# Kernel tuning notes

Measured on AMD Instinct MI355X. Metric: run time of the kernel, lower is better.

The kernel has to match this reference:

```python
import jax, jax.numpy as jnp
import numpy as np

N = 524288          # total atoms (sorted by degree)
E = 1433600         # total directed bonds
B, L = 16384, 32    # molecules x atoms-per-molecule (B*L == N)
NODE, EDGE, H, OUT = 64, 16, 128, 128
N0 = 8192           # number of degree-0 atoms
DEG_COUNTS = {1: 65536, 2: 131072, 3: 196608, 4: 98304, 5: 24576}
BN_EPS = 1e-5


def setup_inputs() -> dict:
    key = jax.random.key(0)
    ks = jax.random.split(key, 24)
    inp = {}
    inp["node_feat"] = jax.random.normal(ks[0], (N, NODE), jnp.float32)
    inp["edge_feat"] = jax.random.normal(ks[1], (E, EDGE), jnp.float32)
    i = 2
    for d in (1, 2, 3, 4, 5):
        n_d = DEG_COUNTS[d]
        inp[f"nbr_node_d{d}"] = jax.random.randint(ks[i], (n_d, d), 0, N, jnp.int32); i += 1
        inp[f"nbr_edge_d{d}"] = jax.random.randint(ks[i], (n_d, d), 0, E, jnp.int32); i += 1
    inp["atom_index"] = jnp.arange(B * L, dtype=jnp.int32).reshape(B, L)

    def lin(k, o, fan_in):
        return jax.random.normal(k, (o, fan_in), jnp.float32) / np.sqrt(fan_in).astype(np.float32)

    inp["out_W0"] = lin(ks[12], OUT, NODE); inp["out_b0"] = jnp.zeros((OUT,), jnp.float32)
    inp["out_W1"] = lin(ks[13], OUT, H);    inp["out_b1"] = jnp.zeros((OUT,), jnp.float32)
    inp["out_W2"] = lin(ks[14], OUT, H);    inp["out_b2"] = jnp.zeros((OUT,), jnp.float32)
    inp["conv0_selfW"] = lin(ks[15], H, NODE)
    inp["conv0_degW"] = jax.random.normal(ks[16], (5, H, NODE + EDGE), jnp.float32) / np.sqrt(NODE + EDGE).astype(np.float32)
    inp["conv0_bias"] = jnp.zeros((1, H), jnp.float32)
    inp["conv1_selfW"] = lin(ks[17], H, H)
    inp["conv1_degW"] = jax.random.normal(ks[18], (5, H, H + EDGE), jnp.float32) / np.sqrt(H + EDGE).astype(np.float32)
    inp["conv1_bias"] = jnp.zeros((1, H), jnp.float32)
    return inp


def _graph_degree_conv(node_repr, edge_repr, selfW, degW, bias, nbr_nodes, nbr_edges):
    out_size = selfW.shape[0]
    # degree 0: zero neighbor contribution
    parts = [jnp.zeros((N0, out_size), node_repr.dtype)]
    for di, d in enumerate((1, 2, 3, 4, 5)):
        nn_rep = node_repr[nbr_nodes[di]]          # [n_d, d, node]
        ee_rep = edge_repr[nbr_edges[di]]          # [n_d, d, edge]
        summed = jnp.concatenate([nn_rep.sum(1), ee_rep.sum(1)], axis=-1)  # [n_d, node+edge]
        parts.append(summed @ degW[di].T)          # per-degree linear (no bias)
    neighbor_repr = jnp.concatenate(parts, axis=0)  # nodes sorted by degree -> aligned
    act = node_repr @ selfW.T + neighbor_repr + bias
    # BatchNorm1d(affine=False), training-mode batch stats (biased variance)
    mean = act.mean(0)
    var = act.var(0)
    act = (act - mean) / jnp.sqrt(var + BN_EPS)
    return jax.nn.relu(act)


def reference(node_feat, edge_feat,
              nbr_node_d1, nbr_edge_d1, nbr_node_d2, nbr_edge_d2,
              nbr_node_d3, nbr_edge_d3, nbr_node_d4, nbr_edge_d4,
              nbr_node_d5, nbr_edge_d5, atom_index,
              out_W0, out_b0, out_W1, out_b1, out_W2, out_b2,
              conv0_selfW, conv0_degW, conv0_bias,
              conv1_selfW, conv1_degW, conv1_bias):
    nbr_nodes = (nbr_node_d1, nbr_node_d2, nbr_node_d3, nbr_node_d4, nbr_node_d5)
    nbr_edges = (nbr_edge_d1, nbr_edge_d2, nbr_edge_d3, nbr_edge_d4, nbr_edge_d5)

    x = node_feat
    acc = jax.nn.softmax(x @ out_W0.T + out_b0, axis=1)
    x = _graph_degree_conv(x, edge_feat, conv0_selfW, conv0_degW, conv0_bias, nbr_nodes, nbr_edges)
    acc = acc + jax.nn.softmax(x @ out_W1.T + out_b1, axis=1)
    x = _graph_degree_conv(x, edge_feat, conv1_selfW, conv1_degW, conv1_bias, nbr_nodes, nbr_edges)
    acc = acc + jax.nn.softmax(x @ out_W2.T + out_b2, axis=1)
    # scatter per-atom activations into [batch, max_len, OUT]
    return acc[atom_index]
```

## Files before the change

### kernel.cpp

```cpp
#include <hip/hip_runtime.h>
#include <math.h>


typedef short  short8   __attribute__((ext_vector_type(8)));
typedef unsigned short ushort8v __attribute__((ext_vector_type(8)));
typedef float  f32x4    __attribute__((ext_vector_type(4)));
typedef unsigned int u32;

static constexpr int  N_ATOMS = 524288;
static constexpr long NROWCOL = (long)N_ATOMS * 128;
static constexpr int  NBLK    = N_ATOMS / 64;

__device__ __forceinline__ ushort f2bf(float x) {
    unsigned u = __float_as_uint(x);
    return (ushort)((u + 0x7fffu + ((u >> 16) & 1u)) >> 16);
}
__device__ __forceinline__ float bf2f(ushort h) {
    return __uint_as_float(((unsigned)h) << 16);
}

__device__ __forceinline__ void gload_lds16(const ushort* g, ushort* l) {
    __builtin_amdgcn_global_load_lds(
        (const __attribute__((address_space(1))) u32*)g,
        (__attribute__((address_space(3))) u32*)l, 16, 0, 0);
}

__device__ __forceinline__ void seg_of(long r, int& d, long& off) {
    if      (r < 73728)  { d = 1; off = 8192;  }
    else if (r < 204800) { d = 2; off = 73728; }
    else if (r < 401408) { d = 3; off = 204800;}
    else if (r < 499712) { d = 4; off = 401408;}
    else                 { d = 5; off = 499712;}
}

__device__ __forceinline__ uint4 pack8(const float v[8]) {
    uint4 w;
    w.x = f2bf(v[0]) | ((unsigned)f2bf(v[1]) << 16);
    w.y = f2bf(v[2]) | ((unsigned)f2bf(v[3]) << 16);
    w.z = f2bf(v[4]) | ((unsigned)f2bf(v[5]) << 16);
    w.w = f2bf(v[6]) | ((unsigned)f2bf(v[7]) << 16);
    return w;
}
__device__ __forceinline__ short8 pack8s(const float v[8]) {
    short8 o;
#pragma unroll
    for (int e = 0; e < 8; ++e) o[e] = (short)f2bf(v[e]);
    return o;
}

__global__ __launch_bounds__(256)
void esum_kernel(const float* __restrict__ edge_feat,
                 const int* __restrict__ ne1, const int* __restrict__ ne2,
                 const int* __restrict__ ne3, const int* __restrict__ ne4,
                 const int* __restrict__ ne5, ushort* __restrict__ esumb)
{
    const long t = (long)blockIdx.x * 256 + threadIdx.x;
    const long r = 8192 + (t >> 1);
    const int  h = (int)(t & 1);
    int d; long off; seg_of(r, d, off);
    const int* ne = (d==1)?ne1:(d==2)?ne2:(d==3)?ne3:(d==4)?ne4:ne5;
    const long i0 = (r - off) * d;
    float v[8] = {0,0,0,0,0,0,0,0};
    for (int j = 0; j < d; ++j) {
        const long e = ne[i0 + j];
        const float4* p = (const float4*)(edge_feat + e * 16 + h * 8);
        const float4 a = p[0], b = p[1];
        v[0]+=a.x; v[1]+=a.y; v[2]+=a.z; v[3]+=a.w;
        v[4]+=b.x; v[5]+=b.y; v[6]+=b.z; v[7]+=b.w;
    }
    *(uint4*)(esumb + (r - 8192) * 16 + h * 8) = pack8(v);
}

__global__ void wprep(const float* __restrict__ src, ushort* __restrict__ dst,
                      int rows, int Ks, int Kd)
{
    const int i = blockIdx.x * 256 + threadIdx.x;
    if (i >= rows * Kd) return;
    const int r = i / Kd, c = i % Kd;
    dst[i] = f2bf(c < Ks ? src[r * Ks + c] : 0.f);
}

__global__ void wprep_img(const float* __restrict__ src, ushort* __restrict__ dst, int K)
{
    const int i = blockIdx.x * 256 + threadIdx.x;
    if (i >= 128 * K) return;
    const int row = i / K, col = i % K;
    dst[(col >> 3) * 1024 + row * 8 + (col & 7)] = f2bf(src[i]);
}

template<int NG, bool F32, bool BN>
__device__ __forceinline__ void stage_rows(const void* Xv, long r0,
                                           ushort* __restrict__ Ab,
                                           const float* __restrict__ statsL)
{
    for (int t = threadIdx.x; t < 64 * NG; t += 256) {
        const int row = t / NG, g = t % NG;
        const long gr = r0 + row;
        float v[8];
        if (F32) {
            const float4* p = (const float4*)((const float*)Xv + gr * (long)(NG * 8) + g * 8);
            const float4 a = p[0], b = p[1];
            v[0]=a.x; v[1]=a.y; v[2]=a.z; v[3]=a.w;
            v[4]=b.x; v[5]=b.y; v[6]=b.z; v[7]=b.w;
        } else {
            const ushort8v u = *(const ushort8v*)((const ushort*)Xv + gr * (long)(NG * 8) + g * 8);
#pragma unroll
            for (int e = 0; e < 8; ++e) v[e] = bf2f(u[e]);
        }
        if (BN) {
            const int c0 = g * 8;
#pragma unroll
            for (int e = 0; e < 8; ++e)
                v[e] = fmaxf(0.f, (v[e] - statsL[c0 + e]) * statsL[128 + c0 + e]);
        }
        ((uint4*)Ab)[row * NG + (g ^ (row & 7))] = pack8(v);
    }
}

template<int NGL, int NST, int NGN, bool F32, bool BN>
__device__ __forceinline__ void stage_gather(const void* Xv,
                                             const ushort* __restrict__ esumb,
                                             const int* __restrict__ nnl, int d,
                                             long r0, ushort* __restrict__ Ab,
                                             const float* __restrict__ statsL)
{
    for (int t = threadIdx.x; t < 64 * NST; t += 256) {
        const int row = t / NST, g = t % NST;
        float v[8] = {0,0,0,0,0,0,0,0};
        if (g < NGN) {
            const int c0 = g * 8;
            for (int j = 0; j < d; ++j) {
                const long idx = nnl[row * d + j];
                if (F32) {
                    const float4* p = (const float4*)((const float*)Xv + idx * (long)(NGN * 8) + c0);
                    const float4 a = p[0], b = p[1];
                    v[0]+=a.x; v[1]+=a.y; v[2]+=a.z; v[3]+=a.w;
                    v[4]+=b.x; v[5]+=b.y; v[6]+=b.z; v[7]+=b.w;
                } else {
                    const ushort8v u = *(const ushort8v*)((const ushort*)Xv + idx * (long)(NGN * 8) + c0);
#pragma unroll
                    for (int e = 0; e < 8; ++e) {
                        float x = bf2f(u[e]);
                        if (BN) x = fmaxf(0.f, (x - statsL[c0 + e]) * statsL[128 + c0 + e]);
                        v[e] += x;
                    }
                }
            }
        } else if (g < NGN + 2) {
            const long er = r0 + row - 8192;
            const ushort8v u = *(const ushort8v*)(esumb + er * 16 + (g - NGN) * 8);
#pragma unroll
            for (int e = 0; e < 8; ++e) v[e] = bf2f(u[e]);
        }
        ((uint4*)Ab)[row * NGL + (g ^ (row & 7))] = pack8(v);
    }
}

template<int KS, int NG>
__device__ __forceinline__ void mfma_lds(const ushort* __restrict__ Ab,
                                         const ushort* __restrict__ Wb, int KP,
                                         int wc, f32x4 acc[4][2])
{
    const int lane = threadIdx.x & 63;
    const int lg = lane >> 4, lr = lane & 15;
#pragma unroll
    for (int ks = 0; ks < KS; ++ks) {
        short8 B0 = *(const short8*)(Wb + (long)(wc + lr) * KP + ks * 32 + 8 * lg);
        short8 B1 = *(const short8*)(Wb + (long)(wc + 16 + lr) * KP + ks * 32 + 8 * lg);
        const int gk = ks * 4 + lg;
#pragma unroll
        for (int m = 0; m < 4; ++m) {
            const int row = 16 * m + lr;
            const short8 a = *(const short8*)(Ab + (row * NG + (gk ^ (row & 7))) * 8);
            acc[m][0] = __builtin_amdgcn_mfma_f32_16x16x32_bf16(a, B0, acc[m][0], 0, 0, 0);
            acc[m][1] = __builtin_amdgcn_mfma_f32_16x16x32_bf16(a, B1, acc[m][1], 0, 0, 0);
        }
    }
}

template<int K1, bool A1F32, bool BNIN, int NGL2, int NST2, int NGN2, int KS2, int KP2>
__global__ __launch_bounds__(256, 2)
void conv_kernel(const void* __restrict__ X, const ushort* __restrict__ Wb1,
                 const ushort* __restrict__ Wb2base,
                 const int* __restrict__ nn1, const int* __restrict__ nn2,
                 const int* __restrict__ nn3, const int* __restrict__ nn4,
                 const int* __restrict__ nn5,
                 const ushort* __restrict__ esumb, const float* __restrict__ cbias,
                 const float* __restrict__ stats_in,
                 ushort* __restrict__ act_out, float* __restrict__ part)
{
    constexpr int NG1 = K1 / 8;
    constexpr int KS1 = K1 / 32;
    constexpr int NGMAX = (NGL2 > NG1) ? NGL2 : NG1;
    __shared__ uint4 AbV[64 * NGMAX];
    __shared__ int   nnl[320];
    __shared__ float statsL[256];
    ushort* Ab = (ushort*)AbV;

    const long r0 = (long)blockIdx.x * 64;
    const int wid = threadIdx.x >> 6, lane = threadIdx.x & 63;
    const int lg = lane >> 4, lr = lane & 15, wc = wid * 32;

    if (BNIN)
        for (int t = threadIdx.x; t < 256; t += 256) statsL[t] = stats_in[t];

    int d = 0;
    const bool has2 = (r0 >= 8192);
    if (has2) {
        long off; seg_of(r0, d, off);
        const int* nn = (d==1)?nn1:(d==2)?nn2:(d==3)?nn3:(d==4)?nn4:nn5;
        const long i0 = (r0 - off) * d;
        for (int t = threadIdx.x; t < 64 * d; t += 256) nnl[t] = nn[i0 + t];
    }
    __syncthreads();

    stage_rows<NG1, A1F32, BNIN>(X, r0, Ab, statsL);
    __syncthreads();
    f32x4 acc[4][2] = {};
    mfma_lds<KS1, NG1>(Ab, Wb1, K1, wc, acc);

    if (has2) {
        __syncthreads();
        stage_gather<NGL2, NST2, NGN2, A1F32, BNIN>(X, esumb, nnl, d, r0, Ab, statsL);
        __syncthreads();
        const ushort* Wb2 = Wb2base + (long)(d - 1) * 128 * KP2;
        mfma_lds<KS2, NGL2>(Ab, Wb2, KP2, wc, acc);
    }

#pragma unroll
    for (int n = 0; n < 2; ++n) {
        const float bv = cbias[wc + n * 16 + lr];
#pragma unroll
        for (int m = 0; m < 4; ++m)
#pragma unroll
            for (int j = 0; j < 4; ++j) acc[m][n][j] += bv;
    }
#pragma unroll
    for (int m = 0; m < 4; ++m)
#pragma unroll
        for (int j = 0; j < 4; ++j) {
            const long row = r0 + 16 * m + 4 * lg + j;
#pragma unroll
            for (int n = 0; n < 2; ++n)
                act_out[row * 128 + wc + n * 16 + lr] = f2bf(acc[m][n][j]);
        }
#pragma unroll
    for (int n = 0; n < 2; ++n) {
        float s = 0.f, q = 0.f;
#pragma unroll
        for (int m = 0; m < 4; ++m)
#pragma unroll
            for (int j = 0; j < 4; ++j) { const float v = acc[m][n][j]; s += v; q += v * v; }
        s += __shfl_xor(s, 16); s += __shfl_xor(s, 32);
        q += __shfl_xor(q, 16); q += __shfl_xor(q, 32);
        if (lane < 16) {
            part[(long)blockIdx.x * 256 + wc + n * 16 + lr]       = s;
            part[(long)blockIdx.x * 256 + 128 + wc + n * 16 + lr] = q;
        }
    }
}

__global__ __launch_bounds__(256)
void bn_finalize(const float* __restrict__ part, float* __restrict__ stats)
{
    const int c = blockIdx.x;
    float s = 0.f, q = 0.f;
    for (int b = threadIdx.x; b < NBLK; b += 256) {
        s += part[(long)b * 256 + c];
        q += part[(long)b * 256 + 128 + c];
    }
#pragma unroll
    for (int o = 1; o < 64; o <<= 1) { s += __shfl_xor(s, o); q += __shfl_xor(q, o); }
    __shared__ float rs[4], rq[4];
    const int wid = threadIdx.x >> 6;
    if ((threadIdx.x & 63) == 0) { rs[wid] = s; rq[wid] = q; }
    __syncthreads();
    if (threadIdx.x == 0) {
        s = rs[0] + rs[1] + rs[2] + rs[3];
        q = rq[0] + rq[1] + rq[2] + rq[3];
        const float mean = s * (1.0f / N_ATOMS);
        const float var  = q * (1.0f / N_ATOMS) - mean * mean;
        stats[c]       = mean;
        stats[128 + c] = 1.0f / sqrtf(var + 1e-5f);
    }
}

__device__ __forceinline__ void mfma8_img(const ushort* __restrict__ Wl, int base,
                                          int ks, int lg, int lr,
                                          short8 af, f32x4 (&acc)[8])
{
    const int a0 = base + (ks * 4 + lg) * 1024 + lr * 8;
#pragma unroll
    for (int n = 0; n < 8; ++n) {
        const short8 bf = *(const short8*)(Wl + a0 + n * 128);
        acc[n] = __builtin_amdgcn_mfma_f32_16x16x32_bf16(af, bf, acc[n], 0, 0, 0);
    }
}

__device__ __forceinline__ short8 cvt_bn(short8 u, int k0, const float* __restrict__ sl)
{
    float v[8];
#pragma unroll
    for (int e = 0; e < 8; ++e)
        v[e] = fmaxf(0.f, (bf2f((ushort)u[e]) - sl[k0 + e]) * sl[128 + k0 + e]);
    return pack8s(v);
}

__device__ __forceinline__ void softmax_accum(f32x4 (&acc)[8],
                                              const float* __restrict__ bias,
                                              int lr, f32x4 (&oacc)[8])
{
    float bb[8];
#pragma unroll
    for (int n = 0; n < 8; ++n) bb[n] = bias[n * 16 + lr];
#pragma unroll
    for (int j = 0; j < 4; ++j) {
        float mx = -1e30f;
#pragma unroll
        for (int n = 0; n < 8; ++n) { acc[n][j] += bb[n]; mx = fmaxf(mx, acc[n][j]); }
        mx = fmaxf(mx, __shfl_xor(mx, 1));
        mx = fmaxf(mx, __shfl_xor(mx, 2));
        mx = fmaxf(mx, __shfl_xor(mx, 4));
        mx = fmaxf(mx, __shfl_xor(mx, 8));
        float s = 0.f;
#pragma unroll
        for (int n = 0; n < 8; ++n) {
            const float e = __expf(acc[n][j] - mx);
            acc[n][j] = e; s += e;
        }
        s += __shfl_xor(s, 1); s += __shfl_xor(s, 2);
        s += __shfl_xor(s, 4); s += __shfl_xor(s, 8);
        const float inv = 1.0f / s;
#pragma unroll
        for (int n = 0; n < 8; ++n) oacc[n][j] += acc[n][j] * inv;
    }
}

__global__ __launch_bounds__(256, 2)
void out_kernel(const float* __restrict__ node, const ushort* __restrict__ act0b,
                const ushort* __restrict__ act1b, const ushort* __restrict__ wimg,
                const float* __restrict__ b0, const float* __restrict__ b1,
                const float* __restrict__ b2,
                const float* __restrict__ stats0, const float* __restrict__ stats1,
                float* __restrict__ out)
{
    __shared__ ushort Wlds[24576];
    __shared__ float sl[512];

    const int wid = threadIdx.x >> 6, lane = threadIdx.x & 63;
    const int lg = lane >> 4, lr = lane & 15;
    const long rA = (long)blockIdx.x * 64 + wid * 16 + lr;

#pragma unroll
    for (int i = 0; i < 12; ++i) {
        const int c = wid * 12 + i;
        gload_lds16(wimg + c * 512 + lane * 8, &Wlds[c * 512]);
    }
    for (int t = threadIdx.x; t < 512; t += 256)
        sl[t] = (t < 256) ? stats0[t] : stats1[t - 256];

    const float4* n0 = (const float4*)(node + rA * 64 + lg * 8);
    const float4* n1 = (const float4*)(node + rA * 64 + 32 + lg * 8);
    float4 h0a = n0[0], h0b = n0[1];
    float4 h1a = n1[0], h1b = n1[1];
    short8 r1[4];
#pragma unroll
    for (int ks = 0; ks < 4; ++ks)
        r1[ks] = *(const short8*)(act0b + rA * 128 + ks * 32 + lg * 8);

    __syncthreads();

    f32x4 oacc[8] = {};
    f32x4 acc[8] = {};
    {
        const float v0[8] = {h0a.x,h0a.y,h0a.z,h0a.w,h0b.x,h0b.y,h0b.z,h0b.w};
        mfma8_img(Wlds, 0, 0, lg, lr, pack8s(v0), acc);
        const float v1[8] = {h1a.x,h1a.y,h1a.z,h1a.w,h1b.x,h1b.y,h1b.z,h1b.w};
        mfma8_img(Wlds, 0, 1, lg, lr, pack8s(v1), acc);
    }
    short8 r2[4];
#pragma unroll
    for (int ks = 0; ks < 4; ++ks)
        r2[ks] = *(const short8*)(act1b + rA * 128 + ks * 32 + lg * 8);

    softmax_accum(acc, b0, lr, oacc);

    {
#pragma unroll
        for (int n = 0; n < 8; ++n) acc[n] = f32x4{0.f, 0.f, 0.f, 0.f};
#pragma unroll
        for (int ks = 0; ks < 4; ++ks) {
            const int k0 = ks * 32 + lg * 8;
            mfma8_img(Wlds, 8192, ks, lg, lr, cvt_bn(r1[ks], k0, sl), acc);
        }
        softmax_accum(acc, b1, lr, oacc);
    }

    __syncthreads();
#pragma unroll
    for (int i = 0; i < 8; ++i) {
        const int c = wid * 8 + i;
        gload_lds16(wimg + 24576 + c * 512 + lane * 8, &Wlds[8192 + c * 512]);
    }
    __syncthreads();

    {
#pragma unroll
        for (int n = 0; n < 8; ++n) acc[n] = f32x4{0.f, 0.f, 0.f, 0.f};
#pragma unroll
        for (int ks = 0; ks < 4; ++ks) {
            const int k0 = ks * 32 + lg * 8;
            mfma8_img(Wlds, 8192, ks, lg, lr, cvt_bn(r2[ks], k0, sl + 256), acc);
        }
        softmax_accum(acc, b2, lr, oacc);
    }

    const long rC0 = (long)blockIdx.x * 64 + wid * 16;
#pragma unroll
    for (int j = 0; j < 4; ++j) {
        const long row = rC0 + 4 * lg + j;
#pragma unroll
        for (int n = 0; n < 8; ++n)
            out[row * 128 + n * 16 + lr] = oacc[n][j];
    }
}

extern "C" void kernel_launch(void* const* d_in, const int* in_sizes, int n_in,
                              void* d_out, int out_size, void* d_ws, size_t ws_size,
                              hipStream_t stream)
{
    const float* node_feat = (const float*)d_in[0];
    const float* edge_feat = (const float*)d_in[1];
    const int* nn1 = (const int*)d_in[2];  const int* ne1 = (const int*)d_in[3];
    const int* nn2 = (const int*)d_in[4];  const int* ne2 = (const int*)d_in[5];
    const int* nn3 = (const int*)d_in[6];  const int* ne3 = (const int*)d_in[7];
    const int* nn4 = (const int*)d_in[8];  const int* ne4 = (const int*)d_in[9];
    const int* nn5 = (const int*)d_in[10]; const int* ne5 = (const int*)d_in[11];
    const float* W0     = (const float*)d_in[13];
    const float* b0     = (const float*)d_in[14];
    const float* W1     = (const float*)d_in[15];
    const float* b1     = (const float*)d_in[16];
    const float* W2     = (const float*)d_in[17];
    const float* b2     = (const float*)d_in[18];
    const float* selfW0 = (const float*)d_in[19];
    const float* degW0  = (const float*)d_in[20];
    const float* cb0    = (const float*)d_in[21];
    const float* selfW1 = (const float*)d_in[22];
    const float* degW1  = (const float*)d_in[23];
    const float* cb1    = (const float*)d_in[24];

    float*  part   = (float*)d_ws;
    float*  stats0 = part + (long)NBLK * 256;
    float*  stats1 = stats0 + 256;
    ushort* act0b  = (ushort*)(stats1 + 256);
    ushort* act1b  = act0b + NROWCOL;
    ushort* esumb  = act1b + NROWCOL;
    ushort* wb_self0 = esumb + (long)516096 * 16;
    ushort* wb_deg0  = wb_self0 + 128 * 64;
    ushort* wb_self1 = wb_deg0  + 640 * 96;
    ushort* wb_deg1  = wb_self1 + 128 * 128;
    ushort* wimg     = wb_deg1  + 640 * 160;
    const size_t needed = (size_t)((char*)(wimg + 40960) - (char*)d_ws);
    if (ws_size < needed) return;

    wprep<<<(128*64 +255)/256, 256, 0, stream>>>(selfW0, wb_self0, 128, 64, 64);
    wprep<<<(640*96 +255)/256, 256, 0, stream>>>(degW0,  wb_deg0,  640, 80, 96);
    wprep<<<(128*128+255)/256, 256, 0, stream>>>(selfW1, wb_self1, 128, 128, 128);
    wprep<<<(640*160+255)/256, 256, 0, stream>>>(degW1,  wb_deg1,  640, 144, 160);
    wprep_img<<<(128*64 +255)/256, 256, 0, stream>>>(W0, wimg,          64);
    wprep_img<<<(128*128+255)/256, 256, 0, stream>>>(W1, wimg + 8192,  128);
    wprep_img<<<(128*128+255)/256, 256, 0, stream>>>(W2, wimg + 24576, 128);

    esum_kernel<<<4032, 256, 0, stream>>>(edge_feat, ne1, ne2, ne3, ne4, ne5, esumb);

    conv_kernel<64, true, false, 16, 12, 8, 3, 96><<<NBLK, 256, 0, stream>>>(
        node_feat, wb_self0, wb_deg0, nn1, nn2, nn3, nn4, nn5, esumb, cb0, nullptr, act0b, part);
    bn_finalize<<<128, 256, 0, stream>>>(part, stats0);

    conv_kernel<128, false, true, 24, 20, 16, 5, 160><<<NBLK, 256, 0, stream>>>(
        act0b, wb_self1, wb_deg1, nn1, nn2, nn3, nn4, nn5, esumb, cb1, stats0, act1b, part);
    bn_finalize<<<128, 256, 0, stream>>>(part, stats1);

    out_kernel<<<NBLK, 256, 0, stream>>>(node_feat, act0b, act1b, wimg,
        b0, b1, b2, stats0, stats1, (float*)d_out);
}
```

Measured before the change: 572.0 us.

## Materialize BN+ReLU of layer-0 activations in a separate pass instead of per-gather

Adds a standalone bnrelu_pass kernel that applies batch-norm and ReLU to the layer-0 activations once and writes a bf16 buffer. The second conv and the output kernel then read the normalized values directly, so the per-neighbor BN math in the gather and the cvt_bn in out_kernel go away. Bf16 packing also switches to the HIP intrinsic __float22bfloat162_rn. The cost is an extra full read and write of a 128 MB activation buffer plus one more launch, traded against repeated BN work across up to five gathered neighbors per row.

```diff
diff --git a/kernel.cpp b/kernel.cpp
--- a/kernel.cpp
+++ b/kernel.cpp
@@ -1,4 +1,5 @@
 #include <hip/hip_runtime.h>
+#include <hip/hip_bf16.h>
 #include <math.h>
 
 
@@ -11,12 +12,30 @@
 static constexpr long NROWCOL = (long)N_ATOMS * 128;
 static constexpr int  NBLK    = N_ATOMS / 64;
 
+__device__ __forceinline__ float bf2f(ushort h) {
+    return __uint_as_float(((unsigned)h) << 16);
+}
 __device__ __forceinline__ ushort f2bf(float x) {
     unsigned u = __float_as_uint(x);
     return (ushort)((u + 0x7fffu + ((u >> 16) & 1u)) >> 16);
 }
-__device__ __forceinline__ float bf2f(ushort h) {
-    return __uint_as_float(((unsigned)h) << 16);
+
+__device__ __forceinline__ uint4 pack8(const float v[8]) {
+    union { __hip_bfloat162 h2[4]; uint4 u; } c;
+#pragma unroll
+    for (int e = 0; e < 4; ++e)
+        c.h2[e] = __float22bfloat162_rn(make_float2(v[2*e], v[2*e+1]));
+    return c.u;
+}
+__device__ __forceinline__ short8 pack8s(const float v[8]) {
+    union { uint4 u; short8 s; } c;
+    c.u = pack8(v);
+    return c.s;
+}
+__device__ __forceinline__ ushort f2bf1(float x) {
+    union { __hip_bfloat16 b; ushort u; } c;
+    c.b = __float2bfloat16(x);
+    return c.u;
 }
 
 __device__ __forceinline__ void gload_lds16(const ushort* g, ushort* l) {
@@ -31,21 +50,6 @@
     else if (r < 401408) { d = 3; off = 204800;}
     else if (r < 499712) { d = 4; off = 401408;}
     else                 { d = 5; off = 499712;}
-}
-
-__device__ __forceinline__ uint4 pack8(const float v[8]) {
-    uint4 w;
-    w.x = f2bf(v[0]) | ((unsigned)f2bf(v[1]) << 16);
-    w.y = f2bf(v[2]) | ((unsigned)f2bf(v[3]) << 16);
-    w.z = f2bf(v[4]) | ((unsigned)f2bf(v[5]) << 16);
-    w.w = f2bf(v[6]) | ((unsigned)f2bf(v[7]) << 16);
-    return w;
-}
-__device__ __forceinline__ short8 pack8s(const float v[8]) {
-    short8 o;
-#pragma unroll
-    for (int e = 0; e < 8; ++e) o[e] = (short)f2bf(v[e]);
-    return o;
 }
 
 __global__ __launch_bounds__(256)
@@ -88,47 +92,38 @@
     dst[(col >> 3) * 1024 + row * 8 + (col & 7)] = f2bf(src[i]);
 }
 
-template<int NG, bool F32, bool BN>
+template<int NG, bool F32>
 __device__ __forceinline__ void stage_rows(const void* Xv, long r0,
-                                           ushort* __restrict__ Ab,
-                                           const float* __restrict__ statsL)
+                                           ushort* __restrict__ Ab)
 {
     for (int t = threadIdx.x; t < 64 * NG; t += 256) {
         const int row = t / NG, g = t % NG;
         const long gr = r0 + row;
-        float v[8];
+        uint4 w;
         if (F32) {
             const float4* p = (const float4*)((const float*)Xv + gr * (long)(NG * 8) + g * 8);
             const float4 a = p[0], b = p[1];
-            v[0]=a.x; v[1]=a.y; v[2]=a.z; v[3]=a.w;
-            v[4]=b.x; v[5]=b.y; v[6]=b.z; v[7]=b.w;
+            const float v[8] = {a.x,a.y,a.z,a.w,b.x,b.y,b.z,b.w};
+            w = pack8(v);
         } else {
-            const ushort8v u = *(const ushort8v*)((const ushort*)Xv + gr * (long)(NG * 8) + g * 8);
-#pragma unroll
-            for (int e = 0; e < 8; ++e) v[e] = bf2f(u[e]);
-        }
-        if (BN) {
-            const int c0 = g * 8;
-#pragma unroll
-            for (int e = 0; e < 8; ++e)
-                v[e] = fmaxf(0.f, (v[e] - statsL[c0 + e]) * statsL[128 + c0 + e]);
-        }
-        ((uint4*)Ab)[row * NG + (g ^ (row & 7))] = pack8(v);
-    }
-}
-
-template<int NGL, int NST, int NGN, bool F32, bool BN>
+            w = *(const uint4*)((const ushort*)Xv + gr * (long)(NG * 8) + g * 8);
+        }
+        ((uint4*)Ab)[row * NG + (g ^ (row & 7))] = w;
+    }
+}
+
+template<int NGL, int NST, int NGN, bool F32>
 __device__ __forceinline__ void stage_gather(const void* Xv,
                                              const ushort* __restrict__ esumb,
                                              const int* __restrict__ nnl, int d,
-                                             long r0, ushort* __restrict__ Ab,
-                                             const float* __restrict__ statsL)
+                                             long r0, ushort* __restrict__ Ab)
 {
     for (int t = threadIdx.x; t < 64 * NST; t += 256) {
         const int row = t / NST, g = t % NST;
-        float v[8] = {0,0,0,0,0,0,0,0};
+        uint4 w = {0, 0, 0, 0};
         if (g < NGN) {
             const int c0 = g * 8;
+            float v[8] = {0,0,0,0,0,0,0,0};
             for (int j = 0; j < d; ++j) {
                 const long idx = nnl[row * d + j];
                 if (F32) {
@@ -139,20 +134,15 @@
                 } else {
                     const ushort8v u = *(const ushort8v*)((const ushort*)Xv + idx * (long)(NGN * 8) + c0);
 #pragma unroll
-                    for (int e = 0; e < 8; ++e) {
-                        float x = bf2f(u[e]);
-                        if (BN) x = fmaxf(0.f, (x - statsL[c0 + e]) * statsL[128 + c0 + e]);
-                        v[e] += x;
-                    }
+                    for (int e = 0; e < 8; ++e) v[e] += bf2f(u[e]);
                 }
             }
+            w = pack8(v);
         } else if (g < NGN + 2) {
             const long er = r0 + row - 8192;
-            const ushort8v u = *(const ushort8v*)(esumb + er * 16 + (g - NGN) * 8);
-#pragma unroll
-            for (int e = 0; e < 8; ++e) v[e] = bf2f(u[e]);
-        }
-        ((uint4*)Ab)[row * NGL + (g ^ (row & 7))] = pack8(v);
+            w = *(const uint4*)(esumb + er * 16 + (g - NGN) * 8);
+        }
+        ((uint4*)Ab)[row * NGL + (g ^ (row & 7))] = w;
     }
 }
 
@@ -178,7 +168,7 @@
     }
 }
 
-template<int K1, bool A1F32, bool BNIN, int NGL2, int NST2, int NGN2, int KS2, int KP2>
+template<int K1, bool A1F32, int NGL2, int NST2, int NGN2, int KS2, int KP2>
 __global__ __launch_bounds__(256, 2)
 void conv_kernel(const void* __restrict__ X, const ushort* __restrict__ Wb1,
                  const ushort* __restrict__ Wb2base,
@@ -186,7 +176,6 @@
                  const int* __restrict__ nn3, const int* __restrict__ nn4,
                  const int* __restrict__ nn5,
                  const ushort* __restrict__ esumb, const float* __restrict__ cbias,
-                 const float* __restrict__ stats_in,
                  ushort* __restrict__ act_out, float* __restrict__ part)
 {
     constexpr int NG1 = K1 / 8;
@@ -194,15 +183,11 @@
     constexpr int NGMAX = (NGL2 > NG1) ? NGL2 : NG1;
     __shared__ uint4 AbV[64 * NGMAX];
     __shared__ int   nnl[320];
-    __shared__ float statsL[256];
     ushort* Ab = (ushort*)AbV;
 
     const long r0 = (long)blockIdx.x * 64;
     const int wid = threadIdx.x >> 6, lane = threadIdx.x & 63;
     const int lg = lane >> 4, lr = lane & 15, wc = wid * 32;
-
-    if (BNIN)
-        for (int t = threadIdx.x; t < 256; t += 256) statsL[t] = stats_in[t];
 
     int d = 0;
     const bool has2 = (r0 >= 8192);
@@ -214,14 +199,14 @@
     }
     __syncthreads();
 
-    stage_rows<NG1, A1F32, BNIN>(X, r0, Ab, statsL);
+    stage_rows<NG1, A1F32>(X, r0, Ab);
     __syncthreads();
     f32x4 acc[4][2] = {};
     mfma_lds<KS1, NG1>(Ab, Wb1, K1, wc, acc);
 
     if (has2) {
         __syncthreads();
-        stage_gather<NGL2, NST2, NGN2, A1F32, BNIN>(X, esumb, nnl, d, r0, Ab, statsL);
+        stage_gather<NGL2, NST2, NGN2, A1F32>(X, esumb, nnl, d, r0, Ab);
         __syncthreads();
         const ushort* Wb2 = Wb2base + (long)(d - 1) * 128 * KP2;
         mfma_lds<KS2, NGL2>(Ab, Wb2, KP2, wc, acc);
@@ -242,7 +227,7 @@
             const long row = r0 + 16 * m + 4 * lg + j;
 #pragma unroll
             for (int n = 0; n < 2; ++n)
-                act_out[row * 128 + wc + n * 16 + lr] = f2bf(acc[m][n][j]);
+                act_out[row * 128 + wc + n * 16 + lr] = f2bf1(acc[m][n][j]);
         }
 #pragma unroll
     for (int n = 0; n < 2; ++n) {
@@ -285,6 +270,23 @@
     }
 }
 
+__global__ __launch_bounds__(256)
+void bnrelu_pass(const ushort* __restrict__ act, const float* __restrict__ stats,
+                 ushort* __restrict__ xout)
+{
+    __shared__ float sl[256];
+    sl[threadIdx.x] = stats[threadIdx.x];
+    __syncthreads();
+    const long i = (long)blockIdx.x * 256 + threadIdx.x;
+    const int c0 = (int)(i & 15) * 8;
+    const ushort8v u = *(const ushort8v*)((const ushort*)act + i * 8);
+    float v[8];
+#pragma unroll
+    for (int e = 0; e < 8; ++e)
+        v[e] = fmaxf(0.f, (bf2f(u[e]) - sl[c0 + e]) * sl[128 + c0 + e]);
+    *(uint4*)(xout + i * 8) = pack8(v);
+}
+
 __device__ __forceinline__ void mfma8_img(const ushort* __restrict__ Wl, int base,
                                           int ks, int lg, int lr,
                                           short8 af, f32x4 (&acc)[8])
@@ -337,15 +339,14 @@
 }
 
 __global__ __launch_bounds__(256, 2)
-void out_kernel(const float* __restrict__ node, const ushort* __restrict__ act0b,
+void out_kernel(const float* __restrict__ node, const ushort* __restrict__ x1b,
                 const ushort* __restrict__ act1b, const ushort* __restrict__ wimg,
                 const float* __restrict__ b0, const float* __restrict__ b1,
                 const float* __restrict__ b2,
-                const float* __restrict__ stats0, const float* __restrict__ stats1,
-                float* __restrict__ out)
+                const float* __restrict__ stats1, float* __restrict__ out)
 {
     __shared__ ushort Wlds[24576];
-    __shared__ float sl[512];
+    __shared__ float sl[256];
 
     const int wid = threadIdx.x >> 6, lane = threadIdx.x & 63;
     const int lg = lane >> 4, lr = lane & 15;
@@ -356,8 +357,7 @@
         const int c = wid * 12 + i;
         gload_lds16(wimg + c * 512 + lane * 8, &Wlds[c * 512]);
     }
-    for (int t = threadIdx.x; t < 512; t += 256)
-        sl[t] = (t < 256) ? stats0[t] : stats1[t - 256];
+    sl[threadIdx.x] = stats1[threadIdx.x];
 
     const float4* n0 = (const float4*)(node + rA * 64 + lg * 8);
     const float4* n1 = (const float4*)(node + rA * 64 + 32 + lg * 8);
@@ -366,7 +366,7 @@
     short8 r1[4];
 #pragma unroll
     for (int ks = 0; ks < 4; ++ks)
-        r1[ks] = *(const short8*)(act0b + rA * 128 + ks * 32 + lg * 8);
+        r1[ks] = *(const short8*)(x1b + rA * 128 + ks * 32 + lg * 8);
 
     __syncthreads();
 
@@ -389,10 +389,8 @@
 #pragma unroll
         for (int n = 0; n < 8; ++n) acc[n] = f32x4{0.f, 0.f, 0.f, 0.f};
 #pragma unroll
-        for (int ks = 0; ks < 4; ++ks) {
-            const int k0 = ks * 32 + lg * 8;
-            mfma8_img(Wlds, 8192, ks, lg, lr, cvt_bn(r1[ks], k0, sl), acc);
-        }
+        for (int ks = 0; ks < 4; ++ks)
+            mfma8_img(Wlds, 8192, ks, lg, lr, r1[ks], acc);
         softmax_accum(acc, b1, lr, oacc);
     }
 
@@ -410,7 +408,7 @@
 #pragma unroll
         for (int ks = 0; ks < 4; ++ks) {
             const int k0 = ks * 32 + lg * 8;
-            mfma8_img(Wlds, 8192, ks, lg, lr, cvt_bn(r2[ks], k0, sl + 256), acc);
+            mfma8_img(Wlds, 8192, ks, lg, lr, cvt_bn(r2[ks], k0, sl), acc);
         }
         softmax_accum(acc, b2, lr, oacc);
     }
@@ -454,7 +452,8 @@
     float*  stats1 = stats0 + 256;
     ushort* act0b  = (ushort*)(stats1 + 256);
     ushort* act1b  = act0b + NROWCOL;
-    ushort* esumb  = act1b + NROWCOL;
+    ushort* x1b    = act1b + NROWCOL;
+    ushort* esumb  = x1b + NROWCOL;
     ushort* wb_self0 = esumb + (long)516096 * 16;
     ushort* wb_deg0  = wb_self0 + 128 * 64;
     ushort* wb_self1 = wb_deg0  + 640 * 96;
@@ -473,14 +472,15 @@
 
     esum_kernel<<<4032, 256, 0, stream>>>(edge_feat, ne1, ne2, ne3, ne4, ne5, esumb);
 
-    conv_kernel<64, true, false, 16, 12, 8, 3, 96><<<NBLK, 256, 0, stream>>>(
-        node_feat, wb_self0, wb_deg0, nn1, nn2, nn3, nn4, nn5, esumb, cb0, nullptr, act0b, part);
+    conv_kernel<64, true, 16, 12, 8, 3, 96><<<NBLK, 256, 0, stream>>>(
+        node_feat, wb_self0, wb_deg0, nn1, nn2, nn3, nn4, nn5, esumb, cb0, act0b, part);
     bn_finalize<<<128, 256, 0, stream>>>(part, stats0);
-
-    conv_kernel<128, false, true, 24, 20, 16, 5, 160><<<NBLK, 256, 0, stream>>>(
-        act0b, wb_self1, wb_deg1, nn1, nn2, nn3, nn4, nn5, esumb, cb1, stats0, act1b, part);
+    bnrelu_pass<<<(int)(NROWCOL / 8 / 256), 256, 0, stream>>>(act0b, stats0, x1b);
+
+    conv_kernel<128, false, 24, 20, 16, 5, 160><<<NBLK, 256, 0, stream>>>(
+        x1b, wb_self1, wb_deg1, nn1, nn2, nn3, nn4, nn5, esumb, cb1, act1b, part);
     bn_finalize<<<128, 256, 0, stream>>>(part, stats1);
 
-    out_kernel<<<NBLK, 256, 0, stream>>>(node_feat, act0b, act1b, wimg,
-        b0, b1, b2, stats0, stats1, (float*)d_out);
-}
+    out_kernel<<<NBLK, 256, 0, stream>>>(node_feat, x1b, act1b, wimg,
+        b0, b1, b2, stats1, (float*)d_out);
+}
```

New measurement: 589.7 us. +3.1%, slower.
